# Kernel optimization log

Measured on AMD Instinct MI355X. Metric: run time of the kernel, lower is better.

The kernel has to match this reference:

```python
import jax, jax.numpy as jnp
import numpy as np
from jax import lax

EPS = 1e-5
SLOPE = 0.01  # default leaky_relu negative slope

def _conv1d(x, w):
    # x: [B, Cin, L], w: [Cout, Cin, K]; padding=1 (same for K=3)
    return lax.conv_general_dilated(x, w, window_strides=(1,), padding=[(1, 1)],
                                    dimension_numbers=('NCH', 'OIH', 'NCH'))

def _bn_train(x, gamma, beta, axes):
    # training-mode BatchNorm: batch stats over `axes`, biased variance
    mean = jnp.mean(x, axis=axes, keepdims=True)
    var = jnp.mean(jnp.square(x - mean), axis=axes, keepdims=True)
    shape = [1] * x.ndim
    shape[1] = x.shape[1]
    g = gamma.reshape(shape); b = beta.reshape(shape)
    return (x - mean) * g / jnp.sqrt(var + EPS) + b

def setup_inputs() -> dict:
    key = jax.random.key(0)
    ks = jax.random.split(key, 6)
    d, d2, out_dim = 64, 128, 128
    bs, T, N = 16, 32, 256
    s = 0.05
    return {
        'x': jax.random.normal(ks[0], (bs, T, N, d), jnp.float32),
        'conv1_w': jax.random.normal(ks[1], (d2, d, 3), jnp.float32) * s,
        'bn1_g': jnp.ones((d2,), jnp.float32), 'bn1_b': jnp.zeros((d2,), jnp.float32),
        'conv2_w': jax.random.normal(ks[2], (d2, d2, 3), jnp.float32) * s,
        'bn2_g': jnp.ones((d2,), jnp.float32), 'bn2_b': jnp.zeros((d2,), jnp.float32),
        'map_w': jax.random.normal(ks[3], (d2, d2), jnp.float32) * s,
        'map_b': jnp.zeros((d2,), jnp.float32),
        'theta_w': jax.random.normal(ks[4], (out_dim, d2), jnp.float32) * s,
        'theta_b': jnp.zeros((out_dim,), jnp.float32),
        'bnS_g': jnp.ones((out_dim,), jnp.float32), 'bnS_b': jnp.zeros((out_dim,), jnp.float32),
    }

def reference(x, conv1_w, bn1_g, bn1_b, conv2_w, bn2_g, bn2_b,
              map_w, map_b, theta_w, theta_b, bnS_g, bnS_b):
    bs, T, N, d = x.shape
    d2 = 2 * d
    # ---- Temporal 1D CNN over time, per node ----
    tem = jnp.transpose(x, (0, 2, 1, 3)).reshape(bs * N, T, d)      # [BN, T, d]
    h = jnp.transpose(tem, (0, 2, 1))                               # [BN, d, T]
    h = jax.nn.relu(_bn_train(_conv1d(h, conv1_w), bn1_g, bn1_b, (0, 2)))
    h = jax.nn.relu(_bn_train(_conv1d(h, conv2_w), bn2_g, bn2_b, (0, 2)))  # [BN, 2d, T]
    # faithful raw reshape (mixes channel/time layout exactly like the torch code)
    tem_out = h.reshape(bs, N, T, d2)
    spa = jnp.transpose(tem_out, (0, 2, 1, 3)).reshape(bs * T, N, d2)  # [B', N, 2d]
    # ---- Dot-product graph construction ----
    mapped = jnp.einsum('bnd,ed->bne', spa, map_w) + map_b            # Linear(2d,2d)
    adj = jnp.einsum('bnd,bmd->bnm', mapped, mapped)                  # [B', N, N]
    eye = jnp.eye(N, dtype=adj.dtype)
    adj = jax.nn.leaky_relu(adj - eye * 1e8, SLOPE)
    adj = jax.nn.softmax(adj, axis=-1) + eye
    # ---- MPNN (k=1): theta(A @ X), BN over channels, leaky_relu ----
    agg = jnp.einsum('bnm,bmd->bnd', adj, spa)                        # bmm(A, X)
    out = jnp.einsum('bnd,od->bno', agg, theta_w) + theta_b           # [B', N, out]
    out = jnp.transpose(out, (0, 2, 1))                               # [B', out, N]
    out = _bn_train(out, bnS_g, bnS_b, (0, 2))
    out = jnp.transpose(out, (0, 2, 1))
    return jax.nn.leaky_relu(out, SLOPE)
```

## Files before the change

kernel.cpp:

```cpp
#include <hip/hip_runtime.h>

#define SLOPE 0.01f
#define EPSB 1e-5f
#define INV_CNT (1.0f/131072.0f)

typedef unsigned short u16;
typedef unsigned int u32;
typedef __attribute__((ext_vector_type(8))) short s16x8;
typedef __attribute__((ext_vector_type(4))) float f4;

__device__ float g_stats[3][2][128];
__device__ float g_sb[3][2][128];
__device__ float g_part[2048][256];
__device__ u16 g_w1h[3][128][64];
__device__ u16 g_w1l[3][128][64];
__device__ u16 g_w2h[3][128][128];
__device__ u16 g_w2l[3][128][128];
__device__ u16 g_wmh[128][128];
__device__ u16 g_wml[128][128];
__device__ u16 g_wqh[128][128];
__device__ u16 g_wql[128][128];

__device__ __forceinline__ float lrelu(float x){ return x > 0.f ? x : SLOPE*x; }
__device__ __forceinline__ u16 f2b(float f){
  u32 u = __float_as_uint(f);
  return (u16)((u + 0x7fffu + ((u >> 16) & 1u)) >> 16);
}
__device__ __forceinline__ float b2f(u16 h){ return __uint_as_float(((u32)h) << 16); }
__device__ __forceinline__ u32 pk(float a, float b){ return (u32)f2b(a) | ((u32)f2b(b) << 16); }
__device__ __forceinline__ u32 pkhl(float f){
  u16 h = f2b(f);
  u16 l = f2b(f - b2f(h));
  return (u32)h | ((u32)l << 16);
}
__device__ __forceinline__ float unhl(u32 v){ return b2f((u16)(v & 0xffff)) + b2f((u16)(v >> 16)); }

__global__ void k_zero(){
  int i = blockIdx.x*256 + threadIdx.x;
  if (i < 768) ((float*)g_stats)[i] = 0.f;
}

__global__ void k_reduce(int which){
  const float* base = &g_part[blockIdx.x*128][0];
  int j = threadIdx.x;
  float s = 0.f;
  #pragma unroll 4
  for (int r = 0; r < 128; ++r) s += base[r*256 + j];
  atomicAdd(&((float*)g_stats)[which*256 + j], s);
}

__global__ void k_prepw(const float* __restrict__ w1, const float* __restrict__ w2,
                        const float* __restrict__ mapw, const float* __restrict__ thw){
  int idx = blockIdx.x*256 + threadIdx.x;
  if (idx < 24576){
    int kk = idx >> 13, r = idx & 8191, co = r >> 6, ci = r & 63;
    float v = w1[co*192 + ci*3 + kk];
    u16 h = f2b(v);
    g_w1h[kk][co][ci] = h; g_w1l[kk][co][ci] = f2b(v - b2f(h));
  } else if (idx < 73728){
    int j = idx - 24576;
    int kk = j >> 14, r = j & 16383, co = r >> 7, ci = r & 127;
    float v = w2[co*384 + ci*3 + kk];
    u16 h = f2b(v);
    g_w2h[kk][co][ci] = h; g_w2l[kk][co][ci] = f2b(v - b2f(h));
  } else if (idx < 90112){
    int j = idx - 73728;
    float v = mapw[j];
    u16 h = f2b(v);
    ((u16*)g_wmh)[j] = h; ((u16*)g_wml)[j] = f2b(v - b2f(h));
  } else if (idx < 106496){
    int j = idx - 90112;
    float v = thw[j];
    u16 h = f2b(v);
    ((u16*)g_wqh)[j] = h; ((u16*)g_wql)[j] = f2b(v - b2f(h));
  }
}

__global__ void k_finalize(const float* __restrict__ g, const float* __restrict__ bta, int which){
  int c = threadIdx.x;
  float mean = g_stats[which][0][c] * INV_CNT;
  float var  = g_stats[which][1][c] * INV_CNT - mean*mean;
  float sc = g[c] * rsqrtf(var + EPSB);
  g_sb[which][0][c] = sc;
  g_sb[which][1][c] = bta[c] - mean*sc;
}

__global__ __launch_bounds__(256) void k_conv1(const float* __restrict__ x, u16* __restrict__ y1hl){
  __shared__ __align__(16) u16 a0h[2][34][72];
  __shared__ __align__(16) u16 a0l[2][34][72];
  __shared__ __align__(16) u16 w1s[128][72];
  const int bid = blockIdx.x;
  const int bn0 = bid*2;
  const int b = bn0 >> 8, n = bn0 & 255;
  const int tid = threadIdx.x;
  const int w = tid >> 6, l = tid & 63, quad = l >> 4, lm = l & 15;
  f4 acc[2][4];
  #pragma unroll
  for (int i = 0; i < 2; ++i)
    #pragma unroll
    for (int j = 0; j < 4; ++j) acc[i][j] = (f4)0.f;

  {
    int nn = tid >> 7, rem = tid & 127, t = rem >> 2, ci0 = (rem & 3)*16;
    const float* px = x + ((b*32 + t)*256 + n + nn)*64 + ci0;
    u16 hh[16], ll[16];
    #pragma unroll
    for (int j = 0; j < 4; ++j){
      float4 v = *(const float4*)(px + 4*j);
      float vv[4] = {v.x, v.y, v.z, v.w};
      #pragma unroll
      for (int e = 0; e < 4; ++e){
        u16 h = f2b(vv[e]);
        hh[4*j+e] = h; ll[4*j+e] = f2b(vv[e] - b2f(h));
      }
    }
    *(uint4*)&a0h[nn][t+1][ci0]   = *(uint4*)&hh[0];
    *(uint4*)&a0h[nn][t+1][ci0+8] = *(uint4*)&hh[8];
    *(uint4*)&a0l[nn][t+1][ci0]   = *(uint4*)&ll[0];
    *(uint4*)&a0l[nn][t+1][ci0+8] = *(uint4*)&ll[8];
  }
  for (int u = tid; u < 288; u += 256){
    int a = u / 144, rr = u % 144, r = rr / 36, cw = rr % 36;
    u32* base = a ? (u32*)&a0l[r>>1][(r&1)*33][0] : (u32*)&a0h[r>>1][(r&1)*33][0];
    base[cw] = 0u;
  }

  for (int kk = 0; kk < 3; ++kk){
    __syncthreads();
    { int co = tid >> 1, c0 = (tid & 1)*32;
      #pragma unroll
      for (int j = 0; j < 4; ++j)
        *(uint4*)&w1s[co][c0 + 8*j] = *(const uint4*)&g_w1h[kk][co][c0 + 8*j];
    }
    __syncthreads();
    #pragma unroll
    for (int s = 0; s < 2; ++s){
      int ci0 = s*32 + quad*8;
      s16x8 af[2], bh[4], bl[4];
      #pragma unroll
      for (int i = 0; i < 2; ++i) af[i] = *(s16x8*)&w1s[(2*w+i)*16 + lm][ci0];
      #pragma unroll
      for (int nt = 0; nt < 4; ++nt){
        bh[nt] = *(s16x8*)&a0h[nt>>1][(nt&1)*16 + lm + kk][ci0];
        bl[nt] = *(s16x8*)&a0l[nt>>1][(nt&1)*16 + lm + kk][ci0];
      }
      #pragma unroll
      for (int i = 0; i < 2; ++i)
        #pragma unroll
        for (int nt = 0; nt < 4; ++nt){
          acc[i][nt] = __builtin_amdgcn_mfma_f32_16x16x32_bf16(af[i], bh[nt], acc[i][nt], 0, 0, 0);
          acc[i][nt] = __builtin_amdgcn_mfma_f32_16x16x32_bf16(af[i], bl[nt], acc[i][nt], 0, 0, 0);
        }
    }
    __syncthreads();
    { int co = tid >> 1, c0 = (tid & 1)*32;
      #pragma unroll
      for (int j = 0; j < 4; ++j)
        *(uint4*)&w1s[co][c0 + 8*j] = *(const uint4*)&g_w1l[kk][co][c0 + 8*j];
    }
    __syncthreads();
    #pragma unroll
    for (int s = 0; s < 2; ++s){
      int ci0 = s*32 + quad*8;
      s16x8 af[2], bh[4];
      #pragma unroll
      for (int i = 0; i < 2; ++i) af[i] = *(s16x8*)&w1s[(2*w+i)*16 + lm][ci0];
      #pragma unroll
      for (int nt = 0; nt < 4; ++nt) bh[nt] = *(s16x8*)&a0h[nt>>1][(nt&1)*16 + lm + kk][ci0];
      #pragma unroll
      for (int i = 0; i < 2; ++i)
        #pragma unroll
        for (int nt = 0; nt < 4; ++nt)
          acc[i][nt] = __builtin_amdgcn_mfma_f32_16x16x32_bf16(af[i], bh[nt], acc[i][nt], 0, 0, 0);
    }
  }
  #pragma unroll
  for (int i = 0; i < 2; ++i){
    int co0 = (2*w+i)*16 + quad*4;
    float s0=0,s1=0,s2=0,s3=0,q0=0,q1=0,q2=0,q3=0;
    #pragma unroll
    for (int nt = 0; nt < 4; ++nt){
      f4 a = acc[i][nt];
      int nn = nt >> 1, t = (nt & 1)*16 + lm;
      uint4 p;
      p.x = pkhl(a.x); p.y = pkhl(a.y); p.z = pkhl(a.z); p.w = pkhl(a.w);
      *(uint4*)&y1hl[(((bn0+nn)*32 + t)*128 + co0)*2] = p;
      s0+=a.x; s1+=a.y; s2+=a.z; s3+=a.w;
      q0+=a.x*a.x; q1+=a.y*a.y; q2+=a.z*a.z; q3+=a.w*a.w;
    }
    #pragma unroll
    for (int m = 1; m < 16; m <<= 1){
      s0+=__shfl_xor(s0,m); s1+=__shfl_xor(s1,m); s2+=__shfl_xor(s2,m); s3+=__shfl_xor(s3,m);
      q0+=__shfl_xor(q0,m); q1+=__shfl_xor(q1,m); q2+=__shfl_xor(q2,m); q3+=__shfl_xor(q3,m);
    }
    if (lm == 0){
      f4 sv = {s0,s1,s2,s3}, qv = {q0,q1,q2,q3};
      *(f4*)&g_part[bid][co0]       = sv;
      *(f4*)&g_part[bid][128 + co0] = qv;
    }
  }
}

__global__ __launch_bounds__(256) void k_conv2(const u16* __restrict__ y1hl, u16* __restrict__ spa){
  __shared__ __align__(16) u16 a1s[2][34][136];
  __shared__ __align__(16) u16 w2s[128][136];
  const int bid = blockIdx.x;
  const int bn0 = bid*2;
  const int b = bn0 >> 8, n = bn0 & 255;
  const int tid = threadIdx.x;
  const int w = tid >> 6, l = tid & 63, quad = l >> 4, lm = l & 15;
  f4 acc2[4][2];
  #pragma unroll
  for (int mt = 0; mt < 4; ++mt)
    #pragma unroll
    for (int i = 0; i < 2; ++i) acc2[mt][i] = (f4)0.f;

  {
    int nn = tid >> 7, rem = tid & 127, t = rem >> 2, ci0 = (rem & 3)*32;
    const u16* py = y1hl + (((bn0+nn)*32 + t)*128)*2;
    #pragma unroll
    for (int j = 0; j < 4; ++j){
      uint4 va = *(const uint4*)&py[(ci0 + 8*j)*2];
      uint4 vb = *(const uint4*)&py[(ci0 + 8*j + 4)*2];
      u32 vv[8] = {va.x, va.y, va.z, va.w, vb.x, vb.y, vb.z, vb.w};
      u16 oo[8];
      #pragma unroll
      for (int e = 0; e < 8; ++e){
        int ci = ci0 + 8*j + e;
        float f = fmaxf(fmaf(unhl(vv[e]), g_sb[0][0][ci], g_sb[0][1][ci]), 0.f);
        oo[e] = f2b(f);
      }
      *(uint4*)&a1s[nn][t+1][ci0 + 8*j] = *(uint4*)&oo[0];
    }
  }
  for (int u = tid; u < 272; u += 256){
    int r = u/68, cw = u%68;
    ((u32*)&a1s[r>>1][(r&1)*33][0])[cw] = 0u;
  }

  for (int kk = 0; kk < 3; ++kk){
    #pragma unroll
    for (int pass = 0; pass < 2; ++pass){
      __syncthreads();
      { int co = tid >> 1, c0 = (tid & 1)*64;
        const u16* src = pass ? &g_w2l[kk][co][0] : &g_w2h[kk][co][0];
        #pragma unroll
        for (int j = 0; j < 8; ++j)
          *(uint4*)&w2s[co][c0 + 8*j] = *(const uint4*)&src[c0 + 8*j];
      }
      __syncthreads();
      #pragma unroll
      for (int s = 0; s < 4; ++s){
        int ci0 = s*32 + quad*8;
        s16x8 ax[4], bw[2];
        #pragma unroll
        for (int mt = 0; mt < 4; ++mt) ax[mt] = *(s16x8*)&a1s[mt>>1][(mt&1)*16 + lm + kk][ci0];
        #pragma unroll
        for (int i = 0; i < 2; ++i) bw[i] = *(s16x8*)&w2s[(2*w+i)*16 + lm][ci0];
        #pragma unroll
        for (int mt = 0; mt < 4; ++mt)
          #pragma unroll
          for (int i = 0; i < 2; ++i)
            acc2[mt][i] = __builtin_amdgcn_mfma_f32_16x16x32_bf16(ax[mt], bw[i], acc2[mt][i], 0, 0, 0);
      }
    }
  }
  #pragma unroll
  for (int i = 0; i < 2; ++i){
    int co = (2*w+i)*16 + lm;
    float s = 0.f, q = 0.f;
    #pragma unroll
    for (int mt = 0; mt < 4; ++mt){
      f4 a = acc2[mt][i];
      int off0 = co*32 + (mt&1)*16 + quad*4;
      int tp = off0 >> 7, cp = off0 & 127;
      int row = (b*32 + tp)*256 + (n + (mt>>1));
      uint2 p; p.x = pk(a.x, a.y); p.y = pk(a.z, a.w);
      *(uint2*)&spa[row*128 + cp] = p;
      s += a.x + a.y + a.z + a.w;
      q += a.x*a.x + a.y*a.y + a.z*a.z + a.w*a.w;
    }
    s += __shfl_xor(s, 16); s += __shfl_xor(s, 32);
    q += __shfl_xor(q, 16); q += __shfl_xor(q, 32);
    if (l < 16){
      g_part[bid][co]       = s;
      g_part[bid][128 + co] = q;
    }
  }
}

__global__ void k_act(u16* __restrict__ spa){
  int idx = blockIdx.x*256 + threadIdx.x;
  int flat = idx*8;
  int cp0 = flat & 127;
  int row = flat >> 7;
  int bpp = row >> 8;
  int tp = bpp & 31;
  int c = (tp*128 + cp0) >> 5;
  float sc = g_sb[1][0][c], bi = g_sb[1][1][c];
  uint4 v = *(uint4*)(spa + flat);
  u16 h[8]; *(uint4*)&h[0] = v;
  u16 o[8];
  #pragma unroll
  for (int i = 0; i < 8; ++i) o[i] = f2b(fmaxf(fmaf(b2f(h[i]), sc, bi), 0.f));
  *(uint4*)(spa + flat) = *(uint4*)&o[0];
}

__global__ __launch_bounds__(256) void k_gemm128b(const u16* __restrict__ A,
                                                  const float* __restrict__ bvec,
                                                  float* __restrict__ outp,
                                                  int wsel, int do_stats){
  __shared__ __align__(16) u16 As[64][136];
  __shared__ __align__(16) u16 Ws[128][136];
  const u16* Wh = wsel ? &g_wqh[0][0] : &g_wmh[0][0];
  const u16* Wl = wsel ? &g_wql[0][0] : &g_wml[0][0];
  const int bid = blockIdx.x;
  const int rowbase = bid * 64;
  const int tid = threadIdx.x;
  const int w = tid >> 6, l = tid & 63, quad = l >> 4, lm = l & 15;
  f4 acc[2][4];
  #pragma unroll
  for (int i = 0; i < 2; ++i)
    #pragma unroll
    for (int rt = 0; rt < 4; ++rt) acc[i][rt] = (f4)0.f;

  { int r = tid >> 2, c0 = (tid & 3)*32;
    #pragma unroll
    for (int j = 0; j < 4; ++j)
      *(uint4*)&As[r][c0 + 8*j] = *(const uint4*)&A[(rowbase + r)*128 + c0 + 8*j];
  }
  #pragma unroll
  for (int pass = 0; pass < 2; ++pass){
    if (pass) __syncthreads();
    { int e = tid >> 1, c0 = (tid & 1)*64;
      const u16* src = (pass ? Wl : Wh) + e*128;
      #pragma unroll
      for (int j = 0; j < 8; ++j)
        *(uint4*)&Ws[e][c0 + 8*j] = *(const uint4*)&src[c0 + 8*j];
    }
    __syncthreads();
    #pragma unroll
    for (int s = 0; s < 4; ++s){
      int k0 = s*32 + quad*8;
      s16x8 aw[2], ba[4];
      #pragma unroll
      for (int i = 0; i < 2; ++i) aw[i] = *(s16x8*)&Ws[(2*w+i)*16 + lm][k0];
      #pragma unroll
      for (int rt = 0; rt < 4; ++rt) ba[rt] = *(s16x8*)&As[rt*16 + lm][k0];
      #pragma unroll
      for (int i = 0; i < 2; ++i)
        #pragma unroll
        for (int rt = 0; rt < 4; ++rt)
          acc[i][rt] = __builtin_amdgcn_mfma_f32_16x16x32_bf16(aw[i], ba[rt], acc[i][rt], 0, 0, 0);
    }
    if (!pass) __syncthreads();
  }
  #pragma unroll
  for (int i = 0; i < 2; ++i){
    int e0 = (2*w+i)*16 + quad*4;
    f4 bv = *(const f4*)&bvec[e0];
    f4 sv = (f4)0.f, qv = (f4)0.f;
    #pragma unroll
    for (int rt = 0; rt < 4; ++rt){
      int row = rowbase + rt*16 + lm;
      f4 o = acc[i][rt] + bv;
      *(f4*)&outp[row*128 + e0] = o;
      sv += o; qv += o*o;
    }
    if (do_stats){
      #pragma unroll
      for (int m = 1; m < 16; m <<= 1){
        sv.x+=__shfl_xor(sv.x,m); sv.y+=__shfl_xor(sv.y,m); sv.z+=__shfl_xor(sv.z,m); sv.w+=__shfl_xor(sv.w,m);
        qv.x+=__shfl_xor(qv.x,m); qv.y+=__shfl_xor(qv.y,m); qv.z+=__shfl_xor(qv.z,m); qv.w+=__shfl_xor(qv.w,m);
      }
      if (lm == 0){
        *(f4*)&g_part[bid][e0]       = sv;
        *(f4*)&g_part[bid][128 + e0] = qv;
      }
    }
  }
}

__global__ __launch_bounds__(256) void k_adjagg(const float* __restrict__ mapped,
                                                const u16* __restrict__ spa,
                                                u16* __restrict__ agg){
  __shared__ __align__(16) char smem[44032];
  u16 (*mbh)[40]   = (u16(*)[40])(smem);
  u16 (*mbl)[40]   = (u16(*)[40])(smem + 20480);
  u16 (*Ps)[264]   = (u16(*)[264])(smem);
  u16 (*spasT)[40] = (u16(*)[40])(smem + 33792);
  const int bp = blockIdx.x >> 2;
  const int nt = blockIdx.x & 3;
  const int tid = threadIdx.x;
  const int w = tid >> 6, l = tid & 63, quad = l >> 4, lm = l & 15;

  f4 sacc[16];
  #pragma unroll
  for (int ct = 0; ct < 16; ++ct) sacc[ct] = (f4)0.f;

  for (int dc = 0; dc < 4; ++dc){
    __syncthreads();
    { int m = tid;
      const float* pm = mapped + (bp*256 + m)*128 + dc*32;
      u16 hh[32], ll[32];
      #pragma unroll
      for (int j = 0; j < 8; ++j){
        float4 v = *(const float4*)(pm + 4*j);
        float vv[4] = {v.x, v.y, v.z, v.w};
        #pragma unroll
        for (int e = 0; e < 4; ++e){
          u16 h = f2b(vv[e]);
          hh[4*j+e] = h; ll[4*j+e] = f2b(vv[e] - b2f(h));
        }
      }
      #pragma unroll
      for (int j = 0; j < 4; ++j){
        *(uint4*)&mbh[m][8*j] = *(uint4*)&hh[8*j];
        *(uint4*)&mbl[m][8*j] = *(uint4*)&ll[8*j];
      }
    }
    __syncthreads();
    s16x8 amh = *(s16x8*)&mbh[nt*64 + w*16 + lm][quad*8];
    s16x8 aml = *(s16x8*)&mbl[nt*64 + w*16 + lm][quad*8];
    #pragma unroll
    for (int ct = 0; ct < 16; ++ct){
      s16x8 bmh = *(s16x8*)&mbh[ct*16 + lm][quad*8];
      s16x8 bml = *(s16x8*)&mbl[ct*16 + lm][quad*8];
      sacc[ct] = __builtin_amdgcn_mfma_f32_16x16x32_bf16(amh, bmh, sacc[ct], 0, 0, 0);
      sacc[ct] = __builtin_amdgcn_mfma_f32_16x16x32_bf16(amh, bml, sacc[ct], 0, 0, 0);
      sacc[ct] = __builtin_amdgcn_mfma_f32_16x16x32_bf16(aml, bmh, sacc[ct], 0, 0, 0);
    }
  }
  __syncthreads();

  #pragma unroll
  for (int r = 0; r < 4; ++r){
    int rowg = nt*64 + w*16 + quad*4 + r;
    float v[16]; float mx = -3.0e38f;
    #pragma unroll
    for (int ct = 0; ct < 16; ++ct){
      float t = sacc[ct][r];
      if (ct*16 + lm == rowg) t -= 1e8f;
      t = lrelu(t);
      v[ct] = t; mx = fmaxf(mx, t);
    }
    #pragma unroll
    for (int m = 1; m < 16; m <<= 1) mx = fmaxf(mx, __shfl_xor(mx, m));
    float sum = 0.f;
    #pragma unroll
    for (int ct = 0; ct < 16; ++ct){ float e = __expf(v[ct] - mx); v[ct] = e; sum += e; }
    #pragma unroll
    for (int m = 1; m < 16; m <<= 1) sum += __shfl_xor(sum, m);
    float inv = 1.0f / sum;
    #pragma unroll
    for (int ct = 0; ct < 16; ++ct)
      Ps[w*16 + quad*4 + r][ct*16 + lm] = f2b(v[ct] * inv);
  }

  f4 acc2[2][4];
  #pragma unroll
  for (int i = 0; i < 2; ++i)
    #pragma unroll
    for (int rt = 0; rt < 4; ++rt) acc2[i][rt] = (f4)0.f;

  for (int mc = 0; mc < 8; ++mc){
    __syncthreads();
    { int ml = tid >> 3, d0 = (tid & 7)*16;
      const u16* ps = spa + (bp*256 + mc*32 + ml)*128 + d0;
      u16 h[16];
      *(uint4*)&h[0] = *(const uint4*)ps;
      *(uint4*)&h[8] = *(const uint4*)(ps + 8);
      #pragma unroll
      for (int j = 0; j < 16; ++j) spasT[d0 + j][ml] = h[j];
    }
    __syncthreads();
    s16x8 afs[2], bfp[4];
    #pragma unroll
    for (int i = 0; i < 2; ++i) afs[i] = *(s16x8*)&spasT[(2*w+i)*16 + lm][quad*8];
    #pragma unroll
    for (int rt = 0; rt < 4; ++rt) bfp[rt] = *(s16x8*)&Ps[rt*16 + lm][mc*32 + quad*8];
    #pragma unroll
    for (int i = 0; i < 2; ++i)
      #pragma unroll
      for (int rt = 0; rt < 4; ++rt)
        acc2[i][rt] = __builtin_amdgcn_mfma_f32_16x16x32_bf16(afs[i], bfp[rt], acc2[i][rt], 0, 0, 0);
  }
  #pragma unroll
  for (int i = 0; i < 2; ++i){
    int d0 = (2*w+i)*16 + quad*4;
    #pragma unroll
    for (int rt = 0; rt < 4; ++rt){
      int grow = bp*256 + nt*64 + rt*16 + lm;
      uint2 sp = *(const uint2*)&spa[grow*128 + d0];
      f4 a = acc2[i][rt];
      a.x += b2f((u16)(sp.x & 0xffff)); a.y += b2f((u16)(sp.x >> 16));
      a.z += b2f((u16)(sp.y & 0xffff)); a.w += b2f((u16)(sp.y >> 16));
      uint2 p; p.x = pk(a.x, a.y); p.y = pk(a.z, a.w);
      *(uint2*)&agg[grow*128 + d0] = p;
    }
  }
}

__global__ void k_bnout(float* __restrict__ outp){
  int idx = blockIdx.x*256 + threadIdx.x;
  int flat = idx*4;
  int o = flat & 127;
  float4 v = *(const float4*)(outp + flat);
  v.x = lrelu(fmaf(v.x, g_sb[2][0][o+0], g_sb[2][1][o+0]));
  v.y = lrelu(fmaf(v.y, g_sb[2][0][o+1], g_sb[2][1][o+1]));
  v.z = lrelu(fmaf(v.z, g_sb[2][0][o+2], g_sb[2][1][o+2]));
  v.w = lrelu(fmaf(v.w, g_sb[2][0][o+3], g_sb[2][1][o+3]));
  *(float4*)(outp + flat) = v;
}

extern "C" void kernel_launch(void* const* d_in, const int* in_sizes, int n_in,
                              void* d_out, int out_size, void* d_ws, size_t ws_size,
                              hipStream_t stream) {
  const float* x    = (const float*)d_in[0];
  const float* w1   = (const float*)d_in[1];
  const float* bn1g = (const float*)d_in[2];
  const float* bn1b = (const float*)d_in[3];
  const float* w2   = (const float*)d_in[4];
  const float* bn2g = (const float*)d_in[5];
  const float* bn2b = (const float*)d_in[6];
  const float* mapw = (const float*)d_in[7];
  const float* mapb = (const float*)d_in[8];
  const float* thw  = (const float*)d_in[9];
  const float* thb  = (const float*)d_in[10];
  const float* bnSg = (const float*)d_in[11];
  const float* bnSb = (const float*)d_in[12];
  float* outp = (float*)d_out;

  u16* spa = (u16*)d_ws;
  u16* agg = spa + 16777216;

  u16*   y1hl   = (u16*)d_out;
  float* mapped = outp;

  k_zero<<<3, 256, 0, stream>>>();
  k_prepw<<<416, 256, 0, stream>>>(w1, w2, mapw, thw);
  k_conv1<<<2048, 256, 0, stream>>>(x, y1hl);
  k_reduce<<<16, 256, 0, stream>>>(0);
  k_finalize<<<1, 128, 0, stream>>>(bn1g, bn1b, 0);
  k_conv2<<<2048, 256, 0, stream>>>(y1hl, spa);
  k_reduce<<<16, 256, 0, stream>>>(1);
  k_finalize<<<1, 128, 0, stream>>>(bn2g, bn2b, 1);
  k_act<<<8192, 256, 0, stream>>>(spa);
  k_gemm128b<<<2048, 256, 0, stream>>>(spa, mapb, mapped, 0, 0);
  k_adjagg<<<2048, 256, 0, stream>>>(mapped, spa, agg);
  k_gemm128b<<<2048, 256, 0, stream>>>(agg, thb, outp, 1, 1);
  k_reduce<<<16, 256, 0, stream>>>(2);
  k_finalize<<<1, 128, 0, stream>>>(bnSg, bnSb, 2);
  k_bnout<<<16384, 256, 0, stream>>>(outp);
}
```

Before: 452.5 us.

## Emit bf16 hi/lo split mapped tiles from GEMM, remap adjagg blocks, widen agg chunks

```diff
diff --git a/kernel.cpp b/kernel.cpp
--- a/kernel.cpp
+++ b/kernel.cpp
@@ -308,7 +308,7 @@
 
 __global__ __launch_bounds__(256) void k_gemm128b(const u16* __restrict__ A,
                                                   const float* __restrict__ bvec,
-                                                  float* __restrict__ outp,
+                                                  void* __restrict__ outv,
                                                   int wsel, int do_stats){
   __shared__ __align__(16) u16 As[64][136];
   __shared__ __align__(16) u16 Ws[128][136];
@@ -359,38 +359,64 @@
   for (int i = 0; i < 2; ++i){
     int e0 = (2*w+i)*16 + quad*4;
     f4 bv = *(const f4*)&bvec[e0];
-    f4 sv = (f4)0.f, qv = (f4)0.f;
-    #pragma unroll
-    for (int rt = 0; rt < 4; ++rt){
-      int row = rowbase + rt*16 + lm;
-      f4 o = acc[i][rt] + bv;
-      *(f4*)&outp[row*128 + e0] = o;
-      sv += o; qv += o*o;
-    }
-    if (do_stats){
-      #pragma unroll
-      for (int m = 1; m < 16; m <<= 1){
-        sv.x+=__shfl_xor(sv.x,m); sv.y+=__shfl_xor(sv.y,m); sv.z+=__shfl_xor(sv.z,m); sv.w+=__shfl_xor(sv.w,m);
-        qv.x+=__shfl_xor(qv.x,m); qv.y+=__shfl_xor(qv.y,m); qv.z+=__shfl_xor(qv.z,m); qv.w+=__shfl_xor(qv.w,m);
-      }
-      if (lm == 0){
-        *(f4*)&g_part[bid][e0]       = sv;
-        *(f4*)&g_part[bid][128 + e0] = qv;
-      }
-    }
-  }
-}
-
-__global__ __launch_bounds__(256) void k_adjagg(const float* __restrict__ mapped,
+    if (wsel == 0){
+      u16* mh = (u16*)outv;
+      u16* ml = mh + 16777216;
+      int dc = e0 >> 5, ec = e0 & 31;
+      #pragma unroll
+      for (int rt = 0; rt < 4; ++rt){
+        int row = rowbase + rt*16 + lm;
+        int bp = row >> 8, m = row & 255;
+        f4 o = acc[i][rt] + bv;
+        float fv[4] = {o.x, o.y, o.z, o.w};
+        u16 hh[4], ll[4];
+        #pragma unroll
+        for (int e = 0; e < 4; ++e){
+          u16 h = f2b(fv[e]);
+          hh[e] = h; ll[e] = f2b(fv[e] - b2f(h));
+        }
+        int off = ((bp*4 + dc)*256 + m)*32 + ec;
+        *(uint2*)&mh[off] = *(uint2*)&hh[0];
+        *(uint2*)&ml[off] = *(uint2*)&ll[0];
+      }
+    } else {
+      float* outp = (float*)outv;
+      f4 sv = (f4)0.f, qv = (f4)0.f;
+      #pragma unroll
+      for (int rt = 0; rt < 4; ++rt){
+        int row = rowbase + rt*16 + lm;
+        f4 o = acc[i][rt] + bv;
+        *(f4*)&outp[row*128 + e0] = o;
+        sv += o; qv += o*o;
+      }
+      if (do_stats){
+        #pragma unroll
+        for (int m = 1; m < 16; m <<= 1){
+          sv.x+=__shfl_xor(sv.x,m); sv.y+=__shfl_xor(sv.y,m); sv.z+=__shfl_xor(sv.z,m); sv.w+=__shfl_xor(sv.w,m);
+          qv.x+=__shfl_xor(qv.x,m); qv.y+=__shfl_xor(qv.y,m); qv.z+=__shfl_xor(qv.z,m); qv.w+=__shfl_xor(qv.w,m);
+        }
+        if (lm == 0){
+          *(f4*)&g_part[bid][e0]       = sv;
+          *(f4*)&g_part[bid][128 + e0] = qv;
+        }
+      }
+    }
+  }
+}
+
+__global__ __launch_bounds__(256) void k_adjagg(const u16* __restrict__ mh,
+                                                const u16* __restrict__ ml,
                                                 const u16* __restrict__ spa,
                                                 u16* __restrict__ agg){
-  __shared__ __align__(16) char smem[44032];
+  __shared__ __align__(16) char smem[52224];
   u16 (*mbh)[40]   = (u16(*)[40])(smem);
   u16 (*mbl)[40]   = (u16(*)[40])(smem + 20480);
   u16 (*Ps)[264]   = (u16(*)[264])(smem);
-  u16 (*spasT)[40] = (u16(*)[40])(smem + 33792);
-  const int bp = blockIdx.x >> 2;
-  const int nt = blockIdx.x & 3;
+  u16 (*spasT)[72] = (u16(*)[72])(smem + 33792);
+  const int rb = blockIdx.x;
+  const int vb = (rb & 7)*256 + (rb >> 3);
+  const int bp = vb >> 2;
+  const int nt = vb & 3;
   const int tid = threadIdx.x;
   const int w = tid >> 6, l = tid & 63, quad = l >> 4, lm = l & 15;
 
@@ -400,23 +426,15 @@
 
   for (int dc = 0; dc < 4; ++dc){
     __syncthreads();
-    { int m = tid;
-      const float* pm = mapped + (bp*256 + m)*128 + dc*32;
-      u16 hh[32], ll[32];
-      #pragma unroll
-      for (int j = 0; j < 8; ++j){
-        float4 v = *(const float4*)(pm + 4*j);
-        float vv[4] = {v.x, v.y, v.z, v.w};
-        #pragma unroll
-        for (int e = 0; e < 4; ++e){
-          u16 h = f2b(vv[e]);
-          hh[4*j+e] = h; ll[4*j+e] = f2b(vv[e] - b2f(h));
-        }
-      }
-      #pragma unroll
-      for (int j = 0; j < 4; ++j){
-        *(uint4*)&mbh[m][8*j] = *(uint4*)&hh[8*j];
-        *(uint4*)&mbl[m][8*j] = *(uint4*)&ll[8*j];
+    {
+      const u16* srch = mh + ((bp*4 + dc) << 13);
+      const u16* srcl = ml + ((bp*4 + dc) << 13);
+      int m0 = tid >> 2, seg = (tid & 3)*8;
+      #pragma unroll
+      for (int r = 0; r < 4; ++r){
+        int m = m0 + r*64;
+        *(uint4*)&mbh[m][seg] = *(const uint4*)&srch[m*32 + seg];
+        *(uint4*)&mbl[m][seg] = *(const uint4*)&srcl[m*32 + seg];
       }
     }
     __syncthreads();
@@ -463,27 +481,36 @@
     #pragma unroll
     for (int rt = 0; rt < 4; ++rt) acc2[i][rt] = (f4)0.f;
 
-  for (int mc = 0; mc < 8; ++mc){
-    __syncthreads();
-    { int ml = tid >> 3, d0 = (tid & 7)*16;
-      const u16* ps = spa + (bp*256 + mc*32 + ml)*128 + d0;
-      u16 h[16];
-      *(uint4*)&h[0] = *(const uint4*)ps;
-      *(uint4*)&h[8] = *(const uint4*)(ps + 8);
-      #pragma unroll
-      for (int j = 0; j < 16; ++j) spasT[d0 + j][ml] = h[j];
-    }
-    __syncthreads();
-    s16x8 afs[2], bfp[4];
-    #pragma unroll
-    for (int i = 0; i < 2; ++i) afs[i] = *(s16x8*)&spasT[(2*w+i)*16 + lm][quad*8];
-    #pragma unroll
-    for (int rt = 0; rt < 4; ++rt) bfp[rt] = *(s16x8*)&Ps[rt*16 + lm][mc*32 + quad*8];
-    #pragma unroll
-    for (int i = 0; i < 2; ++i)
-      #pragma unroll
-      for (int rt = 0; rt < 4; ++rt)
-        acc2[i][rt] = __builtin_amdgcn_mfma_f32_16x16x32_bf16(afs[i], bfp[rt], acc2[i][rt], 0, 0, 0);
+  for (int mc2 = 0; mc2 < 4; ++mc2){
+    __syncthreads();
+    {
+      int mlo = tid & 63;
+      int db = (tid >> 6)*8;
+      const u16* ps = spa + (bp*256 + mc2*64 + mlo)*128;
+      #pragma unroll
+      for (int r = 0; r < 4; ++r){
+        int d0 = db + r*32;
+        uint4 v = *(const uint4*)(ps + d0);
+        u16 h[8]; *(uint4*)&h[0] = v;
+        #pragma unroll
+        for (int j = 0; j < 8; ++j) spasT[d0+j][mlo] = h[j];
+      }
+    }
+    __syncthreads();
+    #pragma unroll
+    for (int ks = 0; ks < 2; ++ks){
+      int m0 = ks*32 + quad*8;
+      s16x8 afs[2], bfp[4];
+      #pragma unroll
+      for (int i = 0; i < 2; ++i) afs[i] = *(s16x8*)&spasT[(2*w+i)*16 + lm][m0];
+      #pragma unroll
+      for (int rt = 0; rt < 4; ++rt) bfp[rt] = *(s16x8*)&Ps[rt*16 + lm][mc2*64 + m0];
+      #pragma unroll
+      for (int i = 0; i < 2; ++i)
+        #pragma unroll
+        for (int rt = 0; rt < 4; ++rt)
+          acc2[i][rt] = __builtin_amdgcn_mfma_f32_16x16x32_bf16(afs[i], bfp[rt], acc2[i][rt], 0, 0, 0);
+    }
   }
   #pragma unroll
   for (int i = 0; i < 2; ++i){
@@ -534,8 +561,9 @@
   u16* spa = (u16*)d_ws;
   u16* agg = spa + 16777216;
 
-  u16*   y1hl   = (u16*)d_out;
-  float* mapped = outp;
+  u16* y1hl = (u16*)d_out;
+  u16* mh   = (u16*)d_out;
+  u16* ml   = mh + 16777216;
 
   k_zero<<<3, 256, 0, stream>>>();
   k_prepw<<<416, 256, 0, stream>>>(w1, w2, mapw, thw);
@@ -546,9 +574,9 @@
   k_reduce<<<16, 256, 0, stream>>>(1);
   k_finalize<<<1, 128, 0, stream>>>(bn2g, bn2b, 1);
   k_act<<<8192, 256, 0, stream>>>(spa);
-  k_gemm128b<<<2048, 256, 0, stream>>>(spa, mapb, mapped, 0, 0);
-  k_adjagg<<<2048, 256, 0, stream>>>(mapped, spa, agg);
-  k_gemm128b<<<2048, 256, 0, stream>>>(agg, thb, outp, 1, 1);
+  k_gemm128b<<<2048, 256, 0, stream>>>(spa, mapb, (void*)mh, 0, 0);
+  k_adjagg<<<2048, 256, 0, stream>>>(mh, ml, spa, agg);
+  k_gemm128b<<<2048, 256, 0, stream>>>(agg, thb, (void*)outp, 1, 1);
   k_reduce<<<16, 256, 0, stream>>>(2);
   k_finalize<<<1, 128, 0, stream>>>(bnSg, bnSb, 2);
   k_bnout<<<16384, 256, 0, stream>>>(outp);
```

New measurement: 429.5 us. 1.05x faster.
